# Kernel tuning notes

Measured on AMD Instinct MI355X. Metric: run time of the kernel, lower is better.

The kernel has to match this reference:

```python
import jax, jax.numpy as jnp
import numpy as np

HIDDEN = 1024
HEADS = 16
HEAD_DIM = HIDDEN // HEADS


def setup_inputs() -> dict:
    key = jax.random.key(0)
    ks = jax.random.split(key, 8)
    B, S = 2, 2048
    scale = 1.0 / np.sqrt(HIDDEN)
    inp = {
        "hidden_states": jax.random.normal(ks[0], (B, S, HIDDEN), dtype=jnp.float32),
        "attention_mask": jnp.zeros((B, 1, 1, S), dtype=jnp.float32),
        "q_w": jax.random.normal(ks[1], (HIDDEN, HIDDEN), dtype=jnp.float32) * scale,
        "q_b": jnp.zeros((HIDDEN,), dtype=jnp.float32),
        "k_w": jax.random.normal(ks[2], (HIDDEN, HIDDEN), dtype=jnp.float32) * scale,
        "k_b": jnp.zeros((HIDDEN,), dtype=jnp.float32),
        "v_w": jax.random.normal(ks[3], (HIDDEN, HIDDEN), dtype=jnp.float32) * scale,
        "v_b": jnp.zeros((HIDDEN,), dtype=jnp.float32),
    }
    return inp


def _split_heads(x):
    # [B, S, H] -> [B, heads, S, head_dim]
    B, S, _ = x.shape
    return x.reshape(B, S, HEADS, HEAD_DIM).transpose(0, 2, 1, 3)


def reference(hidden_states, attention_mask, q_w, q_b, k_w, k_b, v_w, v_b):
    # Linear projections (torch Linear: x @ W.T + b; here weights stored as [in, out])
    q = _split_heads(hidden_states @ q_w + q_b)  # [B, h, S, d]
    k = _split_heads(hidden_states @ k_w + k_b)
    v = _split_heads(hidden_states @ v_w + v_b)

    scores = jnp.einsum("bhqd,bhkd->bhqk", q, k) / jnp.sqrt(jnp.float32(HEAD_DIM))
    scores = scores + attention_mask  # additive mask, broadcast [B,1,1,S]
    probs = jax.nn.softmax(scores, axis=-1)
    # dropout prob = 0.0 -> identity
    ctx = jnp.einsum("bhqk,bhkd->bhqd", probs, v)  # [B, h, S, d]
    B, _, S, _ = ctx.shape
    ctx = ctx.transpose(0, 2, 1, 3).reshape(B, S, HIDDEN)
    return ctx
```

## Files before the change

### kernel.cpp

```cpp
#include <hip/hip_runtime.h>

typedef __bf16 bf16;
typedef __attribute__((ext_vector_type(8))) __bf16 bf16x8;
typedef __attribute__((ext_vector_type(4))) __bf16 bf16x4;
typedef __attribute__((ext_vector_type(4))) float f32x4;
typedef __attribute__((ext_vector_type(2))) unsigned int uint2v;
typedef __attribute__((ext_vector_type(4))) unsigned int uint4v;

#define MFMA(a, b, c) __builtin_amdgcn_mfma_f32_16x16x32_bf16((a), (b), (c), 0, 0, 0)
#define LOG2E 1.44269504088896340736f

__device__ __forceinline__ bf16x8 cvt8(float4 a, float4 b) {
  bf16x8 r;
  r[0] = (bf16)a.x; r[1] = (bf16)a.y; r[2] = (bf16)a.z; r[3] = (bf16)a.w;
  r[4] = (bf16)b.x; r[5] = (bf16)b.y; r[6] = (bf16)b.z; r[7] = (bf16)b.w;
  return r;
}

__device__ __forceinline__ void stage16(const bf16* g, bf16* l) {
  __builtin_amdgcn_global_load_lds(
      (const __attribute__((address_space(1))) void*)g,
      (__attribute__((address_space(3))) void*)l, 16, 0, 0);
}

__global__ __launch_bounds__(256)
void cvt(const float* __restrict__ hs, const float* __restrict__ qw,
         const float* __restrict__ kw, const float* __restrict__ vw,
         bf16* __restrict__ Xb, bf16* __restrict__ Wt) {
  const int bid = blockIdx.x, tid = threadIdx.x;
  if (bid < 2048) {
    size_t off = (size_t)bid * 2048 + tid * 8;
    float4 x0 = *(const float4*)(hs + off);
    float4 x1 = *(const float4*)(hs + off + 4);
    *(bf16x8*)(Xb + off) = cvt8(x0, x1);
  } else {
    int t = bid - 2048;
    int z = t >> 8, ti = t & 255;
    const float* W = (z == 0) ? qw : (z == 1) ? kw : vw;
    int k0 = (ti >> 4) * 64, n0 = (ti & 15) * 64;
    __shared__ bf16 T[64 * 72];
    #pragma unroll
    for (int i = 0; i < 16; ++i) {
      int e = i * 256 + tid;
      int kr = e >> 6, nc = e & 63;
      T[nc * 72 + kr] = (bf16)W[(size_t)(k0 + kr) * 1024 + n0 + nc];
    }
    __syncthreads();
    #pragma unroll
    for (int i = 0; i < 2; ++i) {
      int e = i * 256 + tid;
      int nr = e >> 3, kg = e & 7;
      *(bf16x8*)(Wt + (size_t)z * 1048576 + (size_t)(n0 + nr) * 1024 + k0 + kg * 8) =
          *(const bf16x8*)&T[nr * 72 + kg * 8];
    }
  }
}

__global__ __launch_bounds__(256, 3)
void qkv_gemm(const bf16* __restrict__ Xb, const bf16* __restrict__ Wt,
              const float* __restrict__ qbias, const float* __restrict__ kbias,
              const float* __restrict__ vbias,
              bf16* __restrict__ qo, bf16* __restrict__ ko, bf16* __restrict__ vo) {
  const int blk = blockIdx.x;
  const int xcd = blk & 7, slot = blk >> 3;
  const int mb = xcd * 4 + slot / 24;
  const int nb = slot % 24;
  const int z = nb >> 3, nbm = nb & 7;
  const bf16* W = Wt + (size_t)z * 1048576;

  const int tid = threadIdx.x;
  const int wave = tid >> 6, lane = tid & 63, quad = lane >> 4, c = lane & 15;
  const int wr = wave >> 1, wc = wave & 1;
  const int lrow = lane >> 3;
  const int lg = (lane & 7) ^ lrow;

  __shared__ bf16 As[128 * 64];
  __shared__ bf16 Bs[128 * 64];

  f32x4 acc[4][4] = {};

  for (int k0 = 0; k0 < 1024; k0 += 64) {
    #pragma unroll
    for (int i = 0; i < 4; ++i) {
      int r = wave * 32 + i * 8;
      stage16(Xb + (size_t)(mb * 128 + r + lrow) * 1024 + k0 + lg * 8, &As[r * 64]);
      stage16(W + (size_t)(nbm * 128 + r + lrow) * 1024 + k0 + lg * 8, &Bs[r * 64]);
    }
    __syncthreads();
    #pragma unroll
    for (int ch = 0; ch < 2; ++ch) {
      bf16x8 af[4];
      #pragma unroll
      for (int rt = 0; rt < 4; ++rt) {
        int row = wr * 64 + rt * 16 + c;
        af[rt] = *(const bf16x8*)&As[row * 64 + ((((ch << 2) | quad) ^ (c & 7)) << 3)];
      }
      #pragma unroll
      for (int nt = 0; nt < 4; ++nt) {
        int row = wc * 64 + nt * 16 + c;
        bf16x8 bfrag = *(const bf16x8*)&Bs[row * 64 + ((((ch << 2) | quad) ^ (c & 7)) << 3)];
        #pragma unroll
        for (int rt = 0; rt < 4; ++rt)
          acc[rt][nt] = MFMA(af[rt], bfrag, acc[rt][nt]);
      }
    }
    __syncthreads();
  }

  const float* bias = (z == 0) ? qbias : (z == 1) ? kbias : vbias;
  float bv[4];
  #pragma unroll
  for (int nt = 0; nt < 4; ++nt)
    bv[nt] = bias[nbm * 128 + wc * 64 + nt * 16 + c];

  if (z == 2) {
    #pragma unroll
    for (int rt = 0; rt < 4; ++rt)
      #pragma unroll
      for (int nt = 0; nt < 4; ++nt) {
        int m0 = mb * 128 + wr * 64 + rt * 16 + 4 * quad;
        int n = nbm * 128 + wc * 64 + nt * 16 + c;
        bf16x4 pk;
        #pragma unroll
        for (int reg = 0; reg < 4; ++reg) pk[reg] = (bf16)(acc[rt][nt][reg] + bv[nt]);
        int b = m0 >> 11, s0 = m0 & 2047, h = n >> 6, d = n & 63;
        *(bf16x4*)&vo[(((size_t)b * 16 + h) * 64 + d) * 2048 + s0] = pk;
      }
  } else {
    bf16* dst = (z == 0) ? qo : ko;
    const float scale = (z == 0) ? 0.125f * LOG2E : 1.0f;
    #pragma unroll
    for (int rt = 0; rt < 4; ++rt)
      #pragma unroll
      for (int nt = 0; nt < 4; ++nt)
        #pragma unroll
        for (int reg = 0; reg < 4; ++reg) {
          float v = (acc[rt][nt][reg] + bv[nt]) * scale;
          int m = mb * 128 + wr * 64 + rt * 16 + 4 * quad + reg;
          int n = nbm * 128 + wc * 64 + nt * 16 + c;
          int b = m >> 11, s = m & 2047, h = n >> 6, d = n & 63;
          dst[(((size_t)b * 16 + h) * 2048 + s) * 64 + d] = (bf16)v;
        }
  }
}

__global__ __launch_bounds__(256, 2)
void attn(const bf16* __restrict__ qg, const bf16* __restrict__ kg,
          const bf16* __restrict__ vtg, const float* __restrict__ mask,
          float* __restrict__ out) {
  const int blk = blockIdx.x;
  const int xcd = blk & 7, slot = blk >> 3;
  const int bh = xcd * 4 + (slot >> 4);
  const int qblk = slot & 15;
  const int b = bh >> 4, h = bh & 15;
  const int tid = threadIdx.x;
  const int wave = tid >> 6, lane = tid & 63, quad = lane >> 4, c = lane & 15;
  const int lrow = lane >> 3, lg = (lane & 7) ^ lrow;

  __shared__ __align__(16) bf16 Ks[3][64 * 64];
  __shared__ __align__(16) bf16 Vs[3][64 * 64];
  __shared__ __align__(16) float Ms[2048];

  const bf16* qb_ = qg + (size_t)bh * 2048 * 64;
  const bf16* kb_ = kg + (size_t)bh * 2048 * 64;
  const bf16* vb_ = vtg + (size_t)bh * 64 * 2048;

  #pragma unroll
  for (int i = 0; i < 2; ++i) {
    int idx = i * 1024 + tid * 4;
    float4 m = *(const float4*)&mask[b * 2048 + idx];
    float4 ms = {m.x * LOG2E, m.y * LOG2E, m.z * LOG2E, m.w * LOG2E};
    *(float4*)&Ms[idx] = ms;
  }

  bf16x8 qf[2][2];
  #pragma unroll
  for (int ct = 0; ct < 2; ++ct)
    #pragma unroll
    for (int ch = 0; ch < 2; ++ch)
      qf[ct][ch] = *(const bf16x8*)(qb_ +
          (size_t)(qblk * 128 + wave * 32 + ct * 16 + c) * 64 + ch * 32 + quad * 8);

  #pragma unroll
  for (int t = 0; t < 2; ++t) {
    #pragma unroll
    for (int i = 0; i < 2; ++i) {
      int r = wave * 16 + i * 8;
      stage16(kb_ + (size_t)(t * 64 + r + lrow) * 64 + lg * 8, &Ks[t][r * 64]);
      stage16(vb_ + (size_t)(r + lrow) * 2048 + t * 64 + lg * 8, &Vs[t][r * 64]);
    }
    __builtin_amdgcn_sched_barrier(0);
  }
  __asm__ volatile("s_waitcnt lgkmcnt(0)" ::: "memory");

  f32x4 o[2][4] = {};
  float lsum[2] = {0.f, 0.f};

  int cur = 0;
  for (int kt = 0; kt < 32; ++kt) {
    if (kt < 31) { __asm__ volatile("s_waitcnt vmcnt(4)" ::: "memory"); }
    else         { __asm__ volatile("s_waitcnt vmcnt(0)" ::: "memory"); }
    __builtin_amdgcn_s_barrier();
    __builtin_amdgcn_sched_barrier(0);

    if (kt < 30) {
      int stg = cur - 1; if (stg < 0) stg = 2;
      #pragma unroll
      for (int i = 0; i < 2; ++i) {
        int r = wave * 16 + i * 8;
        stage16(kb_ + (size_t)((kt + 2) * 64 + r + lrow) * 64 + lg * 8,
                &Ks[stg][r * 64]);
        stage16(vb_ + (size_t)(r + lrow) * 2048 + (kt + 2) * 64 + lg * 8,
                &Vs[stg][r * 64]);
      }
    }
    __builtin_amdgcn_sched_barrier(0);

    f32x4 s[2][4] = {};
    __builtin_amdgcn_s_setprio(1);
    #pragma unroll
    for (int nt = 0; nt < 4; ++nt)
      #pragma unroll
      for (int ch = 0; ch < 2; ++ch) {
        bf16x8 kf = *(const bf16x8*)&Ks[cur][(nt * 16 + c) * 64 +
                                            ((((ch << 2) | quad) ^ (c & 7)) << 3)];
        s[0][nt] = MFMA(kf, qf[0][ch], s[0][nt]);
        s[1][nt] = MFMA(kf, qf[1][ch], s[1][nt]);
      }
    __builtin_amdgcn_s_setprio(0);

    float4 mv[4];
    #pragma unroll
    for (int nt = 0; nt < 4; ++nt)
      mv[nt] = *(const float4*)&Ms[kt * 64 + nt * 16 + 4 * quad];

    bf16x8 pa[2][2];
    #pragma unroll
    for (int ct = 0; ct < 2; ++ct) {
      unsigned int U[4][2];
      #pragma unroll
      for (int nt = 0; nt < 4; ++nt) {
        bf16x4 pk;
        #pragma unroll
        for (int reg = 0; reg < 4; ++reg) {
          float mreg = (reg == 0) ? mv[nt].x : (reg == 1) ? mv[nt].y
                     : (reg == 2) ? mv[nt].z : mv[nt].w;
          float p = __builtin_amdgcn_exp2f(s[ct][nt][reg] + mreg);
          lsum[ct] += p;
          pk[reg] = (bf16)p;
        }
        uint2v uu = __builtin_bit_cast(uint2v, pk);
        U[nt][0] = uu.x; U[nt][1] = uu.y;
      }
      #pragma unroll
      for (int ch = 0; ch < 2; ++ch) {
        unsigned int X0 = U[2 * ch][0],     X1 = U[2 * ch][1];
        unsigned int Y0 = U[2 * ch + 1][0], Y1 = U[2 * ch + 1][1];
        __asm__ volatile("v_permlane32_swap_b32 %0, %1" : "+v"(X0), "+v"(Y0));
        __asm__ volatile("v_permlane32_swap_b32 %0, %1" : "+v"(X1), "+v"(Y1));
        __asm__ volatile("v_permlane16_swap_b32 %0, %1" : "+v"(X0), "+v"(Y0));
        __asm__ volatile("v_permlane16_swap_b32 %0, %1" : "+v"(X1), "+v"(Y1));
        uint4v up = {X0, X1, Y0, Y1};
        pa[ct][ch] = __builtin_bit_cast(bf16x8, up);
      }
    }

    __builtin_amdgcn_s_setprio(1);
    #pragma unroll
    for (int ch = 0; ch < 2; ++ch)
      #pragma unroll
      for (int nt = 0; nt < 4; ++nt) {
        bf16x8 vf = *(const bf16x8*)&Vs[cur][(nt * 16 + c) * 64 +
                                            ((((ch << 2) | quad) ^ (c & 7)) << 3)];
        o[0][nt] = MFMA(vf, pa[0][ch], o[0][nt]);
        o[1][nt] = MFMA(vf, pa[1][ch], o[1][nt]);
      }
    __builtin_amdgcn_s_setprio(0);

    cur = (cur == 2) ? 0 : cur + 1;
  }

  #pragma unroll
  for (int ct = 0; ct < 2; ++ct) {
    float l = lsum[ct];
    l += __shfl_xor(l, 16, 64);
    l += __shfl_xor(l, 32, 64);
    const float inv = 1.0f / l;
    const int srow = qblk * 128 + wave * 32 + ct * 16 + c;
    #pragma unroll
    for (int nt = 0; nt < 4; ++nt) {
      float4 st = { o[ct][nt][0] * inv, o[ct][nt][1] * inv,
                    o[ct][nt][2] * inv, o[ct][nt][3] * inv };
      *(float4*)&out[((size_t)b * 2048 + srow) * 1024 + h * 64 + nt * 16 + 4 * quad] = st;
    }
  }
}

extern "C" void kernel_launch(void* const* d_in, const int* in_sizes, int n_in,
                              void* d_out, int out_size, void* d_ws, size_t ws_size,
                              hipStream_t stream) {
  const float* hs   = (const float*)d_in[0];
  const float* mask = (const float*)d_in[1];
  const float* qw   = (const float*)d_in[2];
  const float* qb   = (const float*)d_in[3];
  const float* kw   = (const float*)d_in[4];
  const float* kb   = (const float*)d_in[5];
  const float* vw   = (const float*)d_in[6];
  const float* vb   = (const float*)d_in[7];
  float* out = (float*)d_out;

  bf16* Xb   = (bf16*)d_ws;
  bf16* Wt   = Xb + (size_t)4096 * 1024;
  bf16* q_ws = Wt + (size_t)3 * 1048576;
  bf16* k_ws = q_ws + (size_t)4096 * 1024;
  bf16* v_ws = k_ws + (size_t)4096 * 1024;

  cvt<<<dim3(2816), 256, 0, stream>>>(hs, qw, kw, vw, Xb, Wt);
  qkv_gemm<<<dim3(768), 256, 0, stream>>>(Xb, Wt, qb, kb, vb, q_ws, k_ws, v_ws);
  attn<<<dim3(512), 256, 0, stream>>>(q_ws, k_ws, v_ws, mask, out);
}
```

Measured before the change: 163.8 us.

## Raise attention occupancy with double-buffered K/V and mask-initialized accumulators

Raises the launch bound from 2 to 4 blocks per SIMD group and shrinks the K/V LDS ring from three stages to two, so more blocks can be resident at once. The prefetch distance drops from two tiles to one, with a full vmcnt(0) wait each iteration. The mask is now loaded as the initial value of the QK^T accumulator, which removes the separate add before exp2. The cost is less latency hiding per block and tighter register limits that may cause spills, in exchange for more waves to hide memory latency.

Result: no change. 167.0 us (+2.0%).

```diff
diff --git a/kernel.cpp b/kernel.cpp
--- a/kernel.cpp
+++ b/kernel.cpp
@@ -144,7 +144,7 @@
   }
 }
 
-__global__ __launch_bounds__(256, 2)
+__global__ __launch_bounds__(256, 4)
 void attn(const bf16* __restrict__ qg, const bf16* __restrict__ kg,
           const bf16* __restrict__ vtg, const float* __restrict__ mask,
           float* __restrict__ out) {
@@ -157,8 +157,8 @@
   const int wave = tid >> 6, lane = tid & 63, quad = lane >> 4, c = lane & 15;
   const int lrow = lane >> 3, lg = (lane & 7) ^ lrow;
 
-  __shared__ __align__(16) bf16 Ks[3][64 * 64];
-  __shared__ __align__(16) bf16 Vs[3][64 * 64];
+  __shared__ __align__(16) bf16 Ks[2][64 * 64];
+  __shared__ __align__(16) bf16 Vs[2][64 * 64];
   __shared__ __align__(16) float Ms[2048];
 
   const bf16* qb_ = qg + (size_t)bh * 2048 * 64;
@@ -182,41 +182,43 @@
           (size_t)(qblk * 128 + wave * 32 + ct * 16 + c) * 64 + ch * 32 + quad * 8);
 
   #pragma unroll
-  for (int t = 0; t < 2; ++t) {
-    #pragma unroll
-    for (int i = 0; i < 2; ++i) {
-      int r = wave * 16 + i * 8;
-      stage16(kb_ + (size_t)(t * 64 + r + lrow) * 64 + lg * 8, &Ks[t][r * 64]);
-      stage16(vb_ + (size_t)(r + lrow) * 2048 + t * 64 + lg * 8, &Vs[t][r * 64]);
-    }
-    __builtin_amdgcn_sched_barrier(0);
+  for (int i = 0; i < 2; ++i) {
+    int r = wave * 16 + i * 8;
+    stage16(kb_ + (size_t)(r + lrow) * 64 + lg * 8, &Ks[0][r * 64]);
+    stage16(vb_ + (size_t)(r + lrow) * 2048 + lg * 8, &Vs[0][r * 64]);
   }
   __asm__ volatile("s_waitcnt lgkmcnt(0)" ::: "memory");
 
   f32x4 o[2][4] = {};
   float lsum[2] = {0.f, 0.f};
 
-  int cur = 0;
   for (int kt = 0; kt < 32; ++kt) {
-    if (kt < 31) { __asm__ volatile("s_waitcnt vmcnt(4)" ::: "memory"); }
-    else         { __asm__ volatile("s_waitcnt vmcnt(0)" ::: "memory"); }
+    const int cur = kt & 1;
+    __asm__ volatile("s_waitcnt vmcnt(0)" ::: "memory");
     __builtin_amdgcn_s_barrier();
     __builtin_amdgcn_sched_barrier(0);
 
-    if (kt < 30) {
-      int stg = cur - 1; if (stg < 0) stg = 2;
+    if (kt < 31) {
       #pragma unroll
       for (int i = 0; i < 2; ++i) {
         int r = wave * 16 + i * 8;
-        stage16(kb_ + (size_t)((kt + 2) * 64 + r + lrow) * 64 + lg * 8,
-                &Ks[stg][r * 64]);
-        stage16(vb_ + (size_t)(r + lrow) * 2048 + (kt + 2) * 64 + lg * 8,
-                &Vs[stg][r * 64]);
+        stage16(kb_ + (size_t)((kt + 1) * 64 + r + lrow) * 64 + lg * 8,
+                &Ks[cur ^ 1][r * 64]);
+        stage16(vb_ + (size_t)(r + lrow) * 2048 + (kt + 1) * 64 + lg * 8,
+                &Vs[cur ^ 1][r * 64]);
       }
     }
     __builtin_amdgcn_sched_barrier(0);
 
-    f32x4 s[2][4] = {};
+    f32x4 s[2][4];
+    #pragma unroll
+    for (int nt = 0; nt < 4; ++nt) {
+      float4 mv = *(const float4*)&Ms[kt * 64 + nt * 16 + 4 * quad];
+      f32x4 sv = {mv.x, mv.y, mv.z, mv.w};
+      s[0][nt] = sv;
+      s[1][nt] = sv;
+    }
+
     __builtin_amdgcn_s_setprio(1);
     #pragma unroll
     for (int nt = 0; nt < 4; ++nt)
@@ -229,11 +231,6 @@
       }
     __builtin_amdgcn_s_setprio(0);
 
-    float4 mv[4];
-    #pragma unroll
-    for (int nt = 0; nt < 4; ++nt)
-      mv[nt] = *(const float4*)&Ms[kt * 64 + nt * 16 + 4 * quad];
-
     bf16x8 pa[2][2];
     #pragma unroll
     for (int ct = 0; ct < 2; ++ct) {
@@ -243,9 +240,7 @@
         bf16x4 pk;
         #pragma unroll
         for (int reg = 0; reg < 4; ++reg) {
-          float mreg = (reg == 0) ? mv[nt].x : (reg == 1) ? mv[nt].y
-                     : (reg == 2) ? mv[nt].z : mv[nt].w;
-          float p = __builtin_amdgcn_exp2f(s[ct][nt][reg] + mreg);
+          float p = __builtin_amdgcn_exp2f(s[ct][nt][reg]);
           lsum[ct] += p;
           pk[reg] = (bf16)p;
         }
@@ -276,8 +271,6 @@
         o[1][nt] = MFMA(vf, pa[1][ch], o[1][nt]);
       }
     __builtin_amdgcn_s_setprio(0);
-
-    cur = (cur == 2) ? 0 : cur + 1;
   }
 
   #pragma unroll
```
